# Kernel optimization log

Hardware: AMD Instinct MI355X
Metric: run time of the kernel (lower is better)

## Reference

```python
import jax, jax.numpy as jnp
import numpy as np

HIDDEN = 16  # hidden_channels; conv outputs 3*HIDDEN gate channels

def setup_inputs() -> dict:
    key = jax.random.key(0)
    k1, k2 = jax.random.split(key)
    inputs = jax.random.normal(k1, (4, 16, 31, 128, 128), dtype=jnp.float32)
    # Conv3d weight (O, I, D, H, W); scaled down so tanh/sigmoid gates are not saturated
    W = jax.random.normal(k2, (3 * HIDDEN, 16, 3, 3, 3), dtype=jnp.float32) * 0.05
    b = jnp.zeros((3 * HIDDEN,), dtype=jnp.float32)
    return {"inputs": inputs, "W": W, "b": b}

def reference(inputs, W, b):
    # conv step: Conv3d with padding=1 (SAME for kernel 3, stride 1)
    gates = jax.lax.conv_general_dilated(
        inputs, W, window_strides=(1, 1, 1), padding='SAME',
        dimension_numbers=('NCDHW', 'OIDHW', 'NCDHW'))
    gates = gates + b[None, :, None, None, None]
    Z, F, O = jnp.split(gates, 3, axis=1)
    Z = jnp.tanh(Z)
    F = jax.nn.sigmoid(F)
    O = jax.nn.sigmoid(O)
    # fo-pooling: sequential linear recurrence over time axis (dim 2)
    Zt = jnp.moveaxis(Z, 2, 0)  # (T, N, C, H, W)
    Ft = jnp.moveaxis(F, 2, 0)
    Ot = jnp.moveaxis(O, 2, 0)
    c0 = jnp.zeros_like(Zt[0])  # c=None at t=0 is equivalent to c0=0

    def step(c, zfo):
        z, f, o = zfo
        c = f * c + (1.0 - f) * z
        return c, o * c

    _, h = jax.lax.scan(step, c0, (Zt, Ft, Ot))
    return jnp.moveaxis(h, 0, 2)  # back to (N, C, T, H, W)
```

## Files before the change

kernel.cpp:

```cpp
#include <hip/hip_runtime.h>


typedef __attribute__((ext_vector_type(8))) short short8;
typedef __attribute__((ext_vector_type(4))) float float4v;

#define TD 31
#define HW (128 * 128)
#define LH 6
#define LW 34
#define UNITS (LH * 2 * LW)
#define NSLOT 3
#define SLOTB (UNITS * 16)
#define WUNITS (14 * 3 * 64)

__device__ __forceinline__ short f2bf(float f) {
    unsigned u = __float_as_uint(f);
    u = (u + 0x7FFFu + ((u >> 16) & 1u)) >> 16;
    return (short)u;
}

__device__ __forceinline__ float frcp(float x) { return __builtin_amdgcn_rcpf(x); }

#define BARRIER() asm volatile("s_waitcnt lgkmcnt(0)\n\ts_barrier" ::: "memory")

__global__ __launch_bounds__(256, 2) void qrnn_mfma3(
    const float* __restrict__ x,
    const float* __restrict__ wt,
    const float* __restrict__ bias,
    float* __restrict__ out)
{
    __shared__ short8 wlds[WUNITS];
    __shared__ short8 ring[NSLOT * UNITS];

    const int tid  = threadIdx.x;
    const int lane = tid & 63;
    const int wv   = tid >> 6;
    const int q    = lane >> 4;
    const int px   = lane & 15;
    const int b    = blockIdx.x;
    const int n    = b >> 7;
    const int h0   = ((b >> 2) & 31) * 4;
    const int w0   = (b & 3) * 32;

    const float* xin = x + (size_t)n * (16 * TD * HW);

    for (int k = 0; k < 11; ++k) {
        int u = tid + k * 256;
        if (u < WUNITS) {
            int l = u & 63, rest = u >> 6;
            int g = rest % 3, s = rest / 3;
            int qq = l >> 4, m = l & 15;
            short8 a;
#pragma unroll
            for (int j = 0; j < 8; ++j) {
                int kk = s * 32 + qq * 8 + j;
                int tap = kk >> 4, ic = kk & 15;
                float v = (tap < 27) ? wt[((size_t)((g * 16 + m) * 16 + ic)) * 27 + tap] : 0.f;
                a[j] = f2bf(v);
            }
            wlds[u] = a;
        }
    }

    int  s_off[2][8];
    bool s_in[2], s_ok[2];
#pragma unroll
    for (int i = 0; i < 2; ++i) {
        int u    = tid + i * 256;
        int uu   = (u < UNITS) ? u : 0;
        int wp   = uu % LW;
        int rest = uu / LW;
        int ck   = rest & 1;
        int hp   = rest >> 1;
        int hh   = h0 + hp - 1;
        int ww   = w0 + wp - 1;
        s_in[i] = (u < UNITS);
        s_ok[i] = s_in[i] && ((unsigned)hh < 128u) && ((unsigned)ww < 128u);
        int hc = hh < 0 ? 0 : (hh > 127 ? 127 : hh);
        int wc = ww < 0 ? 0 : (ww > 127 ? 127 : ww);
#pragma unroll
        for (int j = 0; j < 8; ++j)
            s_off[i][j] = ((ck * 8 + j) * TD) * HW + hc * 128 + wc;
    }

    float rvA[2][8], rvB[2][8];

    auto issue = [&](int tt, float (&rv)[2][8]) {
        const bool tz = ((unsigned)tt >= 31u);
        const int  tc = tz ? 0 : tt;
        const float* basep = xin + (size_t)tc * HW;
#pragma unroll
        for (int i = 0; i < 2; ++i) {
            bool ok = s_ok[i] && !tz;
#pragma unroll
            for (int j = 0; j < 8; ++j) {
                float v = basep[s_off[i][j]];
                rv[i][j] = ok ? v : 0.f;
            }
        }
    };

    auto lds_write = [&](int wu, float (&rv)[2][8]) {
#pragma unroll
        for (int i = 0; i < 2; ++i) {
            if (s_in[i]) {
                short8 v;
#pragma unroll
                for (int j = 0; j < 8; ++j) v[j] = f2bf(rv[i][j]);
                ring[wu + tid + i * 256] = v;
            }
        }
    };

    int roff[14];
#pragma unroll
    for (int s = 0; s < 14; ++s) {
        int T = 2 * s + (q >> 1); if (T > 26) T = 26;
        int kd = T / 9, rr = T - kd * 9, kh = rr / 3, kw = rr - kh * 3;
        roff[s] = (((wv + kh) * 2 + (q & 1)) * LW + px + kw) * 16;
    }
    const int kd4 = q >> 1;

    float4v bv[3];
#pragma unroll
    for (int g = 0; g < 3; ++g)
        bv[g] = (float4v){bias[g * 16 + q * 4 + 0], bias[g * 16 + q * 4 + 1],
                          bias[g * 16 + q * 4 + 2], bias[g * 16 + q * 4 + 3]};

    float* po = out + ((size_t)(n * 16 + q * 4) * TD) * HW
                    + (size_t)(h0 + wv) * 128 + w0 + px;
    float cst[2][4] = {{0.f,0.f,0.f,0.f},{0.f,0.f,0.f,0.f}};

    issue(-1, rvA); lds_write(0,         rvA);
    issue(0,  rvA); lds_write(UNITS,     rvA);
    issue(1,  rvA); lds_write(2 * UNITS, rvA);
    issue(2,  rvA);
    BARRIER();

    auto body = [&](int t, int pk0, int pk1, int pk2, int wu,
                    float (&rvW)[2][8], float (&rvI)[2][8]) {
        issue(t + 3, rvI);

        float4v acc[2][3];
#pragma unroll
        for (int g = 0; g < 3; ++g) { acc[0][g] = bv[g]; acc[1][g] = bv[g]; }

        const int pk[3] = {pk0, pk1, pk2};
        constexpr int kdt[14] = {0,0,0,0, 0 , 1,1,1,1, 2,2,2,2,2};
        const char* ringb = (const char*)ring;
#pragma unroll
        for (int s = 0; s < 14; ++s) {
            int sb = (s == 4) ? (kd4 ? pk1 : pk0) : pk[kdt[s]];
            const short8* bp = (const short8*)(ringb + sb + roff[s]);
            short8 b0 = bp[0];
            short8 b1 = bp[16];
#pragma unroll
            for (int g = 0; g < 3; ++g) {
                short8 wf = wlds[(s * 3 + g) * 64 + lane];
                acc[0][g] = __builtin_amdgcn_mfma_f32_16x16x32_bf16(wf, b0, acc[0][g], 0, 0, 0);
                acc[1][g] = __builtin_amdgcn_mfma_f32_16x16x32_bf16(wf, b1, acc[1][g], 0, 0, 0);
            }
        }
        BARRIER();
        lds_write(wu, rvW);

#pragma unroll
        for (int tile = 0; tile < 2; ++tile) {
#pragma unroll
            for (int r = 0; r < 4; ++r) {
                float az = acc[tile][0][r];
                float af = acc[tile][1][r];
                float ao = acc[tile][2][r];
                float z = 1.f - 2.f * frcp(__expf(2.f * az) + 1.f);
                float f = frcp(1.f + __expf(-af));
                float o = frcp(1.f + __expf(-ao));
                float c = f * cst[tile][r] + (1.f - f) * z;
                cst[tile][r] = c;
                po[(size_t)r * (TD * HW) + tile * 16] = o * c;
            }
        }
        po += HW;
        BARRIER();
    };

    int pk0 = 0, pk1 = SLOTB, pk2 = 2 * SLOTB;
    int wu = 0;
    for (int t = 0; t < 30; t += 2) {
        body(t,     pk0, pk1, pk2, wu,  rvA, rvB);
        int wu1 = (wu == 2 * UNITS) ? 0 : wu + UNITS;
        body(t + 1, pk1, pk2, pk0, wu1, rvB, rvA);
        int t0 = pk0; pk0 = pk2; pk2 = pk1; pk1 = t0;
        wu = (wu1 == 2 * UNITS) ? 0 : wu1 + UNITS;
    }
    body(30, pk0, pk1, pk2, wu, rvA, rvB);
}

extern "C" void kernel_launch(void* const* d_in, const int* in_sizes, int n_in,
                              void* d_out, int out_size, void* d_ws, size_t ws_size,
                              hipStream_t stream) {
    const float* x    = (const float*)d_in[0];
    const float* wt   = (const float*)d_in[1];
    const float* bias = (const float*)d_in[2];
    float* out = (float*)d_out;

    qrnn_mfma3<<<dim3(512), dim3(256), 0, stream>>>(x, wt, bias, out);
}
```

Measured before the change: 292.1 us.

## Use four-slot LDS ring to drop one barrier per timestep

```diff
diff --git a/kernel.cpp b/kernel.cpp
--- a/kernel.cpp
+++ b/kernel.cpp
@@ -9,9 +9,10 @@
 #define LH 6
 #define LW 34
 #define UNITS (LH * 2 * LW)
-#define NSLOT 3
+#define NSLOT 4
 #define SLOTB (UNITS * 16)
 #define WUNITS (14 * 3 * 64)
+#define SMEM_BYTES ((WUNITS + NSLOT * UNITS) * 16)
 
 __device__ __forceinline__ short f2bf(float f) {
     unsigned u = __float_as_uint(f);
@@ -21,16 +22,23 @@
 
 __device__ __forceinline__ float frcp(float x) { return __builtin_amdgcn_rcpf(x); }
 
+__device__ __forceinline__ unsigned cvtpk(float lo, float hi) {
+    unsigned r;
+    asm("v_cvt_pk_bf16_f32 %0, %1, %2" : "=v"(r) : "v"(lo), "v"(hi));
+    return r;
+}
+
 #define BARRIER() asm volatile("s_waitcnt lgkmcnt(0)\n\ts_barrier" ::: "memory")
 
-__global__ __launch_bounds__(256, 2) void qrnn_mfma3(
+__global__ __launch_bounds__(256, 2) void qrnn_mfma4(
     const float* __restrict__ x,
     const float* __restrict__ wt,
     const float* __restrict__ bias,
     float* __restrict__ out)
 {
-    __shared__ short8 wlds[WUNITS];
-    __shared__ short8 ring[NSLOT * UNITS];
+    extern __shared__ short8 smem[];
+    short8* wlds = smem;
+    short8* ring = smem + WUNITS;
 
     const int tid  = threadIdx.x;
     const int lane = tid & 63;
@@ -61,9 +69,16 @@
             wlds[u] = a;
         }
     }
+    {
+        short8 z = (short8)0;
+        for (int k = 0; k < 7; ++k) {
+            int u = tid + k * 256;
+            if (u < NSLOT * UNITS) ring[u] = z;
+        }
+    }
 
     int  s_off[2][8];
-    bool s_in[2], s_ok[2];
+    bool s_ok[2];
 #pragma unroll
     for (int i = 0; i < 2; ++i) {
         int u    = tid + i * 256;
@@ -74,8 +89,7 @@
         int hp   = rest >> 1;
         int hh   = h0 + hp - 1;
         int ww   = w0 + wp - 1;
-        s_in[i] = (u < UNITS);
-        s_ok[i] = s_in[i] && ((unsigned)hh < 128u) && ((unsigned)ww < 128u);
+        s_ok[i] = (u < UNITS) && ((unsigned)hh < 128u) && ((unsigned)ww < 128u);
         int hc = hh < 0 ? 0 : (hh > 127 ? 127 : hh);
         int wc = ww < 0 ? 0 : (ww > 127 ? 127 : ww);
 #pragma unroll
@@ -86,29 +100,32 @@
     float rvA[2][8], rvB[2][8];
 
     auto issue = [&](int tt, float (&rv)[2][8]) {
-        const bool tz = ((unsigned)tt >= 31u);
-        const int  tc = tz ? 0 : tt;
+        const int tc = ((unsigned)tt >= 31u) ? 0 : tt;
         const float* basep = xin + (size_t)tc * HW;
 #pragma unroll
-        for (int i = 0; i < 2; ++i) {
-            bool ok = s_ok[i] && !tz;
-#pragma unroll
-            for (int j = 0; j < 8; ++j) {
-                float v = basep[s_off[i][j]];
-                rv[i][j] = ok ? v : 0.f;
-            }
-        }
+        for (int i = 0; i < 2; ++i)
+#pragma unroll
+            for (int j = 0; j < 8; ++j)
+                rv[i][j] = basep[s_off[i][j]];
     };
 
-    auto lds_write = [&](int wu, float (&rv)[2][8]) {
-#pragma unroll
-        for (int i = 0; i < 2; ++i) {
-            if (s_in[i]) {
-                short8 v;
-#pragma unroll
-                for (int j = 0; j < 8; ++j) v[j] = f2bf(rv[i][j]);
-                ring[wu + tid + i * 256] = v;
-            }
+    auto lds_write = [&](int wu, float (&rv)[2][8], bool tz) {
+        if (!tz) {
+#pragma unroll
+            for (int i = 0; i < 2; ++i) {
+                if (s_ok[i]) {
+                    union { short8 s; unsigned u[4]; } v;
+#pragma unroll
+                    for (int k = 0; k < 4; ++k)
+                        v.u[k] = cvtpk(rv[i][2 * k], rv[i][2 * k + 1]);
+                    ring[wu + tid + i * 256] = v.s;
+                }
+            }
+        } else {
+            short8 z = (short8)0;
+#pragma unroll
+            for (int i = 0; i < 2; ++i)
+                if (s_ok[i]) ring[wu + tid + i * 256] = z;
         }
     };
 
@@ -131,13 +148,13 @@
                     + (size_t)(h0 + wv) * 128 + w0 + px;
     float cst[2][4] = {{0.f,0.f,0.f,0.f},{0.f,0.f,0.f,0.f}};
 
-    issue(-1, rvA); lds_write(0,         rvA);
-    issue(0,  rvA); lds_write(UNITS,     rvA);
-    issue(1,  rvA); lds_write(2 * UNITS, rvA);
-    issue(2,  rvA);
     BARRIER();
-
-    auto body = [&](int t, int pk0, int pk1, int pk2, int wu,
+    issue(0, rvA); lds_write(0 * UNITS, rvA, false);
+    issue(1, rvA); lds_write(1 * UNITS, rvA, false);
+    issue(2, rvA);
+    BARRIER();
+
+    auto body = [&](int t, int r0, int r1, int r2, int r3,
                     float (&rvW)[2][8], float (&rvI)[2][8]) {
         issue(t + 3, rvI);
 
@@ -145,12 +162,12 @@
 #pragma unroll
         for (int g = 0; g < 3; ++g) { acc[0][g] = bv[g]; acc[1][g] = bv[g]; }
 
-        const int pk[3] = {pk0, pk1, pk2};
+        const int pk[3] = {r0, r1, r2};
         constexpr int kdt[14] = {0,0,0,0, 0 , 1,1,1,1, 2,2,2,2,2};
         const char* ringb = (const char*)ring;
 #pragma unroll
         for (int s = 0; s < 14; ++s) {
-            int sb = (s == 4) ? (kd4 ? pk1 : pk0) : pk[kdt[s]];
+            int sb = (s == 4) ? (kd4 ? r1 : r0) : pk[kdt[s]];
             const short8* bp = (const short8*)(ringb + sb + roff[s]);
             short8 b0 = bp[0];
             short8 b1 = bp[16];
@@ -161,8 +178,7 @@
                 acc[1][g] = __builtin_amdgcn_mfma_f32_16x16x32_bf16(wf, b1, acc[1][g], 0, 0, 0);
             }
         }
-        BARRIER();
-        lds_write(wu, rvW);
+        lds_write(r3 >> 4, rvW, t >= 29);
 
 #pragma unroll
         for (int tile = 0; tile < 2; ++tile) {
@@ -183,16 +199,14 @@
         BARRIER();
     };
 
-    int pk0 = 0, pk1 = SLOTB, pk2 = 2 * SLOTB;
-    int wu = 0;
+    int r0 = 3 * SLOTB, r1 = 0, r2 = SLOTB, r3 = 2 * SLOTB;
     for (int t = 0; t < 30; t += 2) {
-        body(t,     pk0, pk1, pk2, wu,  rvA, rvB);
-        int wu1 = (wu == 2 * UNITS) ? 0 : wu + UNITS;
-        body(t + 1, pk1, pk2, pk0, wu1, rvB, rvA);
-        int t0 = pk0; pk0 = pk2; pk2 = pk1; pk1 = t0;
-        wu = (wu1 == 2 * UNITS) ? 0 : wu1 + UNITS;
-    }
-    body(30, pk0, pk1, pk2, wu, rvA, rvB);
+        body(t,     r0, r1, r2, r3, rvA, rvB);
+        body(t + 1, r1, r2, r3, r0, rvB, rvA);
+        int a = r0, c = r1;
+        r0 = r2; r1 = r3; r2 = a; r3 = c;
+    }
+    body(30, r0, r1, r2, r3, rvA, rvB);
 }
 
 extern "C" void kernel_launch(void* const* d_in, const int* in_sizes, int n_in,
@@ -203,5 +217,13 @@
     const float* bias = (const float*)d_in[2];
     float* out = (float*)d_out;
 
-    qrnn_mfma3<<<dim3(512), dim3(256), 0, stream>>>(x, wt, bias, out);
-}
+    static bool configured = false;
+    if (!configured) {
+        hipFuncSetAttribute((const void*)qrnn_mfma4,
+                            hipFuncAttributeMaxDynamicSharedMemorySize,
+                            SMEM_BYTES);
+        configured = true;
+    }
+
+    qrnn_mfma4<<<dim3(512), dim3(256), SMEM_BYTES, stream>>>(x, wt, bias, out);
+}
```

Result: no change. 290.1 us (-0.7%).
